# Kernel optimization log

Measured on AMD Instinct MI355X. Metric: run time of the kernel, lower is better.

Reference implementation:

```python
import jax, jax.numpy as jnp
import numpy as np

NDIM = (256, 256, 256)
NMIN = (-1.0, -1.0, -1.0)
NMAX = (1.0, 1.0, 1.0)
NDELTA = tuple((NMAX[i] - NMIN[i]) / (NDIM[i] - 1.0) for i in range(3))
MIN_DEG, MAX_DEG = 0, 10
ANNEALED_ALPHA = 1.0
EPS = 1e-12


def compute_grad(grid):
    # central differences on the voxel grid with edge padding -> [N, 3]
    g = grid.reshape(NDIM[0], NDIM[1], NDIM[2])
    p = jnp.pad(g, ((1, 1), (1, 1), (1, 1)), mode='edge')
    dx = (p[2:, 1:-1, 1:-1] - p[:-2, 1:-1, 1:-1]) / (2.0 * NDELTA[0])
    dy = (p[1:-1, 2:, 1:-1] - p[1:-1, :-2, 1:-1]) / (2.0 * NDELTA[1])
    dz = (p[1:-1, 1:-1, 2:] - p[1:-1, 1:-1, :-2]) / (2.0 * NDELTA[2])
    return jnp.stack([dx, dy, dz], axis=-1).reshape(-1, 3)


def trilinear3(data, pts):
    # data: [N, 4] flattened voxel features, pts: [B, 3] -> [B, 4]
    x = (pts[..., 0] - NMIN[0]) / NDELTA[0]
    y = (pts[..., 1] - NMIN[1]) / NDELTA[1]
    z = (pts[..., 2] - NMIN[2]) / NDELTA[2]
    x0f = jnp.floor(x); y0f = jnp.floor(y); z0f = jnp.floor(z)
    xd = (x - x0f)[..., None]
    yd = (y - y0f)[..., None]
    zd = (z - z0f)[..., None]
    x0 = jnp.clip(x0f.astype(jnp.int32), 0, NDIM[0] - 1)
    x1 = jnp.clip(x0f.astype(jnp.int32) + 1, 0, NDIM[0] - 1)
    y0 = jnp.clip(y0f.astype(jnp.int32), 0, NDIM[1] - 1)
    y1 = jnp.clip(y0f.astype(jnp.int32) + 1, 0, NDIM[1] - 1)
    z0 = jnp.clip(z0f.astype(jnp.int32), 0, NDIM[2] - 1)
    z1 = jnp.clip(z0f.astype(jnp.int32) + 1, 0, NDIM[2] - 1)
    sYZ, sZ = NDIM[1] * NDIM[2], NDIM[2]
    gat = lambda i, j, k: data[sYZ * i + sZ * j + k]
    c00 = gat(x0, y0, z0) * (1 - xd) + gat(x1, y0, z0) * xd
    c01 = gat(x0, y0, z1) * (1 - xd) + gat(x1, y0, z1) * xd
    c10 = gat(x0, y1, z0) * (1 - xd) + gat(x1, y1, z0) * xd
    c11 = gat(x0, y1, z1) * (1 - xd) + gat(x1, y1, z1) * xd
    c0 = c00 * (1 - yd) + c10 * yd
    c1 = c01 * (1 - yd) + c11 * yd
    return c0 * (1 - zd) + c1 * zd


def annealed_pos_enc(x, alpha):
    # nerfies-style windowed positional encoding with identity concat
    bands = jnp.arange(MIN_DEG, MAX_DEG, dtype=x.dtype)  # [D]
    scales = 2.0 ** bands
    xb = x[..., None, :] * scales[:, None]               # [..., D, 3]
    four = jnp.sin(jnp.stack([xb, xb + 0.5 * jnp.pi], axis=-2))  # [..., D, 2, 3]
    w = jnp.clip(alpha - bands, 0.0, 1.0)
    w = 0.5 * (1.0 - jnp.cos(jnp.pi * w))                # cosine easing window
    four = four * w[:, None, None]
    four = four.reshape(x.shape[:-1] + (-1,))            # [..., D*6]
    return jnp.concatenate([x, four], axis=-1)           # [..., 3 + D*6]


def mlp(feats, w0, b0, w1, b1, w2, b2, w3, b3, wo, bo):
    # net_depth=4, skip_layer=2 -> concat inputs after layer index 2
    h = jax.nn.relu(feats @ w0 + b0)
    h = jax.nn.relu(h @ w1 + b1)
    h = jax.nn.relu(h @ w2 + b2)
    h = jnp.concatenate([h, feats], axis=-1)
    h = jax.nn.relu(h @ w3 + b3)
    return h @ wo + bo


def safe_l2_norm(v):
    return jnp.sqrt(jnp.sum(v * v, axis=-1, keepdims=True) + EPS)


def setup_inputs() -> dict:
    key = jax.random.key(0)
    ks = jax.random.split(key, 8)
    B = 1048576
    N = NDIM[0] * NDIM[1] * NDIM[2]
    x = jax.random.uniform(ks[0], (B, 3), jnp.float32, -1.0, 1.0)
    grid = jax.random.normal(ks[1], (N, 1), jnp.float32)
    glorot = lambda k, fi, fo: jax.random.normal(k, (fi, fo), jnp.float32) * jnp.sqrt(2.0 / (fi + fo))
    return {
        'x': x, 'grid': grid,
        'w0': glorot(ks[2], 63, 128), 'b0': jnp.zeros((128,), jnp.float32),
        'w1': glorot(ks[3], 128, 128), 'b1': jnp.zeros((128,), jnp.float32),
        'w2': glorot(ks[4], 128, 128), 'b2': jnp.zeros((128,), jnp.float32),
        'w3': glorot(ks[5], 191, 128), 'b3': jnp.zeros((128,), jnp.float32),
        'wo': jax.random.normal(ks[6], (128, 3), jnp.float32) * 1e-5,  # output_init normal(1e-5)
        'bo': jnp.zeros((3,), jnp.float32),
    }


def reference(x, grid, w0, b0, w1, b1, w2, b2, w3, b3, wo, bo):
    data = jnp.concatenate([grid, compute_grad(grid)], axis=-1)  # [N, 4]
    ret = trilinear3(data, x)                                    # [B, 4]
    feats = annealed_pos_enc(x[:, None], ANNEALED_ALPHA * MAX_DEG)  # [B, 1, 63]
    raw = mlp(feats, w0, b0, w1, b1, w2, b2, w3, b3, wo, bo)[:, 0]  # [B, 3]
    # residual + direct output: rotate gradient vector by axis-angle raw
    theta = safe_l2_norm(raw)
    e = raw / theta
    cond = ret[..., 1:]
    a = safe_l2_norm(cond)
    v = cond / a
    rot = a * (jnp.cos(theta) * v + jnp.sin(theta) * jnp.cross(e, v)
               + (1.0 - jnp.cos(theta)) * jnp.sum(e * v, axis=-1, keepdims=True) * e)
    return (ret[..., :1], ret[..., 1:], rot)
```

## Files before the change

### kernel.cpp

```cpp
#include <hip/hip_runtime.h>


typedef __attribute__((ext_vector_type(8))) short bf8;
typedef __attribute__((ext_vector_type(4))) float f4;

__device__ __forceinline__ float bf2f(unsigned int u) {
    union { float f; unsigned int i; } v; v.i = u << 16; return v.f;
}
__device__ __forceinline__ unsigned short f2bf(float f) {
    union { float f; unsigned int i; } v; v.f = f;
    unsigned int x = v.i;
    return (unsigned short)((x + 0x7fffu + ((x >> 16) & 1u)) >> 16);
}
__device__ __forceinline__ unsigned int pkbf(float a, float b) {
    unsigned int r;
    asm("v_cvt_pk_bf16_f32 %0, %1, %2" : "=v"(r) : "v"(a), "v"(b));
    return r;
}
__device__ __forceinline__ float gv(const float* __restrict__ g, int i, int j, int k) {
    return g[(i * 256 + j) * 256 + k];
}
__device__ __forceinline__ int featmap(int kp) {
    if (kp < 3) return kp;
    if (kp == 3) return -1;
    const int m = kp - 4, b = m / 6, r = m - 6 * b, d = r >> 1, c = r & 1;
    return 3 + 6 * b + 3 * c + d;
}

#define WS_TOTAL 67584
#define SWZ_BLOCKS 264
#define DG_OFF_SH 131072
#define WS_NEED (262144ull + 16777216ull * 8ull)

__global__ __launch_bounds__(256) void prep(
    const float* __restrict__ g,
    const float* __restrict__ w0, const float* __restrict__ w1,
    const float* __restrict__ w2, const float* __restrict__ w3,
    const float* __restrict__ wo,
    unsigned short* __restrict__ ws, unsigned short* __restrict__ dg,
    int do_dgrid)
{
    const int bid = blockIdx.x;
    if (bid < SWZ_BLOCKS) {
        int idx = bid * 256 + threadIdx.x;
        const float* src; int base, NT, Kact, Nact, ld;
        if (idx < 8192)       { src = w0; base = 0;     NT = 8; Kact = 64;  Nact = 128; ld = 128; }
        else if (idx < 24576) { src = w1; base = 8192;  NT = 8; Kact = 128; Nact = 128; ld = 128; }
        else if (idx < 40960) { src = w2; base = 24576; NT = 8; Kact = 128; Nact = 128; ld = 128; }
        else if (idx < 65536) { src = w3; base = 40960; NT = 8; Kact = 192; Nact = 128; ld = 128; }
        else                  { src = wo; base = 65536; NT = 1; Kact = 128; Nact = 3;   ld = 3;   }
        int local = idx - base;
        int j = local & 7;
        int lane = (local >> 3) & 63;
        int chunk = local >> 9;
        int nt = chunk % NT, kt = chunk / NT;
        int k = kt * 32 + ((lane >> 4) << 3) + j;
        int n = nt * 16 + (lane & 15);
        float v = 0.0f;
        if (k < Kact && n < Nact) {
            int ko = k;
            if (base == 0)            ko = featmap(k);
            else if (base == 40960 && k >= 128) {
                int f = featmap(k - 128);
                ko = (f < 0) ? -1 : 128 + f;
            }
            if (ko >= 0) v = src[ko * ld + n];
        }
        ws[idx] = f2bf(v);
    } else if (do_dgrid) {
        const int t  = (bid - SWZ_BLOCKS) * 256 + threadIdx.x;
        const int k0 = (t & 63) << 2;
        const int j  = (t >> 6) & 255;
        const int i  = t >> 14;
        const float* row = g + (i * 256 + j) * 256;
        const f4 self = *(const f4*)(row + k0);
        const f4 xp = *(const f4*)(g + (min(i + 1, 255) * 256 + j) * 256 + k0);
        const f4 xm = *(const f4*)(g + (max(i - 1, 0)   * 256 + j) * 256 + k0);
        const f4 yp = *(const f4*)(g + (i * 256 + min(j + 1, 255)) * 256 + k0);
        const f4 ym = *(const f4*)(g + (i * 256 + max(j - 1, 0))   * 256 + k0);
        const float zlo = row[max(k0 - 1, 0)];
        const float zhi = row[min(k0 + 4, 255)];
        float zv[6] = {zlo, self[0], self[1], self[2], self[3], zhi};
        unsigned int o[8];
        #pragma unroll
        for (int q = 0; q < 4; ++q) {
            o[q * 2 + 0] = pkbf(self[q], (xp[q] - xm[q]) * 63.75f);
            o[q * 2 + 1] = pkbf((yp[q] - ym[q]) * 63.75f, (zv[q + 2] - zv[q]) * 63.75f);
        }
        unsigned short* dst = dg + (size_t)(((i * 256 + j) * 256 + k0)) * 4;
        *(uint4*)(dst)     = *(const uint4*)(o);
        *(uint4*)(dst + 8) = *(const uint4*)(o + 4);
    }
}

#define WV_SH 6656
#define HSTRIDE 136
#define FSTRIDE 72

template<bool FAST>
__global__ __launch_bounds__(256, 3) void voxmlp(
    const float* __restrict__ x, const float* __restrict__ grid,
    const unsigned short* __restrict__ ws, const unsigned short* __restrict__ dg,
    const float* __restrict__ b0, const float* __restrict__ b1,
    const float* __restrict__ b2, const float* __restrict__ b3,
    const float* __restrict__ bo,
    float* __restrict__ out, int B)
{
    __shared__ unsigned short smem[WV_SH * 4];

    const int lane = threadIdx.x & 63;
    const int wave = threadIdx.x >> 6;
    const int quad = lane >> 4;
    const int lm   = lane & 15;
    unsigned short* bufH = smem + wave * WV_SH;
    unsigned short* fbuf = bufH + 32 * HSTRIDE;

    const int pbase = blockIdx.x * 128 + wave * 32;

    const int p2   = lane & 31;
    const int role = lane >> 5;
    const int pid  = pbase + p2;

    const float px = x[pid * 3 + 0];
    const float py = x[pid * 3 + 1];
    const float pz = x[pid * 3 + 2];

    if (role == 0) {
        const float fx = (px + 1.0f) * 127.5f;
        const float fy = (py + 1.0f) * 127.5f;
        const float fz = (pz + 1.0f) * 127.5f;
        const float fx0 = floorf(fx), fy0 = floorf(fy), fz0 = floorf(fz);
        const float xd = fx - fx0, yd = fy - fy0, zd = fz - fz0;
        const int ix0 = min(max((int)fx0, 0), 255);
        const int iy0 = min(max((int)fy0, 0), 255);
        const int iz0 = min(max((int)fz0, 0), 255);
        const int ix1 = min(ix0 + 1, 255);
        const int iy1 = min(iy0 + 1, 255);
        const int iz1 = min(iz0 + 1, 255);

        float ret0 = 0.f, c1 = 0.f, c2 = 0.f, c3 = 0.f;
        if (FAST) {
            #pragma unroll
            for (int c = 0; c < 8; ++c) {
                const int i = (c & 4) ? ix1 : ix0;
                const int j = (c & 2) ? iy1 : iy0;
                const int k = (c & 1) ? iz1 : iz0;
                const float wgt = ((c & 4) ? xd : 1.0f - xd) *
                                  ((c & 2) ? yd : 1.0f - yd) *
                                  ((c & 1) ? zd : 1.0f - zd);
                const uint2 w = *(const uint2*)(dg + (size_t)((i * 256 + j) * 256 + k) * 4);
                ret0 = fmaf(wgt, bf2f(w.x & 0xffffu), ret0);
                c1   = fmaf(wgt, bf2f(w.x >> 16),     c1);
                c2   = fmaf(wgt, bf2f(w.y & 0xffffu), c2);
                c3   = fmaf(wgt, bf2f(w.y >> 16),     c3);
            }
        } else {
            #pragma unroll
            for (int c = 0; c < 8; ++c) {
                const int i = (c & 4) ? ix1 : ix0;
                const int j = (c & 2) ? iy1 : iy0;
                const int k = (c & 1) ? iz1 : iz0;
                const float wgt = ((c & 4) ? xd : 1.0f - xd) *
                                  ((c & 2) ? yd : 1.0f - yd) *
                                  ((c & 1) ? zd : 1.0f - zd);
                const float v  = gv(grid, i, j, k);
                const float gx = (gv(grid, min(i + 1, 255), j, k) - gv(grid, max(i - 1, 0), j, k)) * 63.75f;
                const float gy = (gv(grid, i, min(j + 1, 255), k) - gv(grid, i, max(j - 1, 0), k)) * 63.75f;
                const float gz = (gv(grid, i, j, min(k + 1, 255)) - gv(grid, i, j, max(k - 1, 0))) * 63.75f;
                ret0 = fmaf(wgt, v,  ret0);
                c1   = fmaf(wgt, gx, c1);
                c2   = fmaf(wgt, gy, c2);
                c3   = fmaf(wgt, gz, c3);
            }
        }
        out[pid] = ret0;
        out[B + pid * 3 + 0] = c1;
        out[B + pid * 3 + 1] = c2;
        out[B + pid * 3 + 2] = c3;
        float* cst = (float*)(fbuf + p2 * FSTRIDE + 64);
        cst[0] = c1; cst[1] = c2; cst[2] = c3;
    } else {
        unsigned int f[32];
        f[0] = pkbf(px, py);
        f[1] = pkbf(pz, 0.0f);
        const float crd[3] = {px, py, pz};
        float s = 1.0f;
        #pragma unroll
        for (int b = 0; b < 10; ++b) {
            #pragma unroll
            for (int d = 0; d < 3; ++d) {
                float sv, cv;
                __sincosf(crd[d] * s, &sv, &cv);
                f[2 + b * 3 + d] = pkbf(sv, cv);
            }
            s *= 2.0f;
        }
        unsigned short* fb = fbuf + p2 * FSTRIDE;
        #pragma unroll
        for (int i = 0; i < 8; ++i)
            *(uint4*)(fb + i * 8) = *(const uint4*)(&f[i * 4]);
    }
    __builtin_amdgcn_s_barrier();

    bf8 af[2][6];
    const int arow0 = lm * HSTRIDE + quad * 8;
    const int frow0 = lm * FSTRIDE + quad * 8;

    auto store_tile = [&](f4 acc, int pt, int ut) {
        uint2 pk;
        pk.x = pkbf(fmaxf(acc[0], 0.f), fmaxf(acc[1], 0.f));
        pk.y = pkbf(fmaxf(acc[2], 0.f), fmaxf(acc[3], 0.f));
        *(uint2*)(bufH + (pt * 16 + lm) * HSTRIDE + ut * 16 + quad * 4) = pk;
    };

    #pragma unroll
    for (int pt = 0; pt < 2; ++pt)
        #pragma unroll
        for (int kt = 0; kt < 2; ++kt)
            af[pt][kt] = *(const bf8*)(fbuf + pt * 16 * FSTRIDE + frow0 + kt * 32);
    #pragma unroll
    for (int ut = 0; ut < 8; ++ut) {
        bf8 wf[2];
        #pragma unroll
        for (int kt = 0; kt < 2; ++kt)
            wf[kt] = *(const bf8*)(ws + 0 + (((kt * 8 + ut) * 64 + lane) << 3));
        const f4 bias = *(const f4*)(b0 + ut * 16 + quad * 4);
        #pragma unroll
        for (int pt = 0; pt < 2; ++pt) {
            f4 acc = bias;
            #pragma unroll
            for (int kt = 0; kt < 2; ++kt)
                acc = __builtin_amdgcn_mfma_f32_16x16x32_bf16(wf[kt], af[pt][kt], acc, 0, 0, 0);
            store_tile(acc, pt, ut);
        }
    }
    __builtin_amdgcn_s_barrier();

    #pragma unroll
    for (int layer = 0; layer < 2; ++layer) {
        const unsigned short* wsl = ws + (layer == 0 ? 8192 : 24576);
        const float* bias_p = (layer == 0) ? b1 : b2;
        #pragma unroll
        for (int pt = 0; pt < 2; ++pt)
            #pragma unroll
            for (int kt = 0; kt < 4; ++kt)
                af[pt][kt] = *(const bf8*)(bufH + pt * 16 * HSTRIDE + arow0 + kt * 32);
        #pragma unroll
        for (int ut = 0; ut < 8; ++ut) {
            bf8 wf[4];
            #pragma unroll
            for (int kt = 0; kt < 4; ++kt)
                wf[kt] = *(const bf8*)(wsl + (((kt * 8 + ut) * 64 + lane) << 3));
            const f4 bias = *(const f4*)(bias_p + ut * 16 + quad * 4);
            #pragma unroll
            for (int pt = 0; pt < 2; ++pt) {
                f4 acc = bias;
                #pragma unroll
                for (int kt = 0; kt < 4; ++kt)
                    acc = __builtin_amdgcn_mfma_f32_16x16x32_bf16(wf[kt], af[pt][kt], acc, 0, 0, 0);
                store_tile(acc, pt, ut);
            }
        }
        __builtin_amdgcn_s_barrier();
    }

    #pragma unroll
    for (int pt = 0; pt < 2; ++pt) {
        #pragma unroll
        for (int kt = 0; kt < 4; ++kt)
            af[pt][kt] = *(const bf8*)(bufH + pt * 16 * HSTRIDE + arow0 + kt * 32);
        #pragma unroll
        for (int kk = 0; kk < 2; ++kk)
            af[pt][4 + kk] = *(const bf8*)(fbuf + pt * 16 * FSTRIDE + frow0 + kk * 32);
    }
    #pragma unroll
    for (int ut = 0; ut < 8; ++ut) {
        bf8 wf[6];
        #pragma unroll
        for (int kt = 0; kt < 6; ++kt)
            wf[kt] = *(const bf8*)(ws + 40960 + (((kt * 8 + ut) * 64 + lane) << 3));
        const f4 bias = *(const f4*)(b3 + ut * 16 + quad * 4);
        #pragma unroll
        for (int pt = 0; pt < 2; ++pt) {
            f4 acc = bias;
            #pragma unroll
            for (int kt = 0; kt < 6; ++kt)
                acc = __builtin_amdgcn_mfma_f32_16x16x32_bf16(wf[kt], af[pt][kt], acc, 0, 0, 0);
            store_tile(acc, pt, ut);
        }
    }
    __builtin_amdgcn_s_barrier();

    #pragma unroll
    for (int pt = 0; pt < 2; ++pt)
        #pragma unroll
        for (int kt = 0; kt < 4; ++kt)
            af[pt][kt] = *(const bf8*)(bufH + pt * 16 * HSTRIDE + arow0 + kt * 32);
    bf8 wf[4];
    #pragma unroll
    for (int kt = 0; kt < 4; ++kt)
        wf[kt] = *(const bf8*)(ws + 65536 + ((kt * 64 + lane) << 3));

    #pragma unroll
    for (int pt = 0; pt < 2; ++pt) {
        f4 acc;
        #pragma unroll
        for (int r = 0; r < 4; ++r) {
            const int u = quad * 4 + r;
            acc[r] = (u < 3) ? bo[u] : 0.0f;
        }
        #pragma unroll
        for (int kt = 0; kt < 4; ++kt)
            acc = __builtin_amdgcn_mfma_f32_16x16x32_bf16(wf[kt], af[pt][kt], acc, 0, 0, 0);

        const int pp = pt * 16 + lm;
        const float* cst = (const float*)(fbuf + pp * FSTRIDE + 64);
        const float g1 = cst[0], g2 = cst[1], g3 = cst[2];
        const float r0 = acc[0], r1 = acc[1], r2 = acc[2];
        const float theta = sqrtf(fmaf(r0, r0, fmaf(r1, r1, r2 * r2)) + 1e-12f);
        const float it = __builtin_amdgcn_rcpf(theta);
        const float e0 = r0 * it, e1 = r1 * it, e2 = r2 * it;
        const float a = sqrtf(fmaf(g1, g1, fmaf(g2, g2, g3 * g3)) + 1e-12f);
        const float ia = __builtin_amdgcn_rcpf(a);
        const float v0 = g1 * ia, v1 = g2 * ia, v2 = g3 * ia;
        float st, ct;
        __sincosf(theta, &st, &ct);
        const float cx = e1 * v2 - e2 * v1;
        const float cy = e2 * v0 - e0 * v2;
        const float cz = e0 * v1 - e1 * v0;
        const float om = (1.0f - ct) * (e0 * v0 + e1 * v1 + e2 * v2);
        if (quad == 0) {
            const int pid2 = pbase + pp;
            out[4 * B + pid2 * 3 + 0] = a * (ct * v0 + st * cx + om * e0);
            out[4 * B + pid2 * 3 + 1] = a * (ct * v1 + st * cy + om * e1);
            out[4 * B + pid2 * 3 + 2] = a * (ct * v2 + st * cz + om * e2);
        }
    }
}

extern "C" void kernel_launch(void* const* d_in, const int* in_sizes, int n_in,
                              void* d_out, int out_size, void* d_ws, size_t ws_size,
                              hipStream_t stream)
{
    const float* x    = (const float*)d_in[0];
    const float* grid = (const float*)d_in[1];
    const float* w0   = (const float*)d_in[2];
    const float* b0   = (const float*)d_in[3];
    const float* w1   = (const float*)d_in[4];
    const float* b1   = (const float*)d_in[5];
    const float* w2   = (const float*)d_in[6];
    const float* b2   = (const float*)d_in[7];
    const float* w3   = (const float*)d_in[8];
    const float* b3   = (const float*)d_in[9];
    const float* wo   = (const float*)d_in[10];
    const float* bo   = (const float*)d_in[11];
    float* out = (float*)d_out;
    unsigned short* ws = (unsigned short*)d_ws;
    unsigned short* dg = ws + DG_OFF_SH;

    const int B = in_sizes[0] / 3;
    const int fast = (ws_size >= WS_NEED) ? 1 : 0;
    const int nprep = fast ? (SWZ_BLOCKS + 16384) : SWZ_BLOCKS;
    prep<<<nprep, 256, 0, stream>>>(grid, w0, w1, w2, w3, wo, ws, dg, fast);
    if (fast)
        voxmlp<true><<<B / 128, 256, 0, stream>>>(x, grid, ws, dg, b0, b1, b2, b3, bo, out, B);
    else
        voxmlp<false><<<B / 128, 256, 0, stream>>>(x, grid, ws, dg, b0, b1, b2, b3, bo, out, B);
}
```

Baseline: 372.2 us.

## Switch MLP matmuls to FP8 MFMA and widen derivative-grid prep per thread

Weights, positional features and hidden activations are now stored as FP8 and fed to the fp8 16x16x32 MFMA instead of bf16. This halves the weight and LDS traffic and lets occupancy rise to 5 waves per SIMD. The tiny output weights are pre-scaled by 8192 to stay in FP8 range and unscaled afterwards. The prep kernel also processes 8 voxels per thread instead of 4. FP8 lowers MLP accuracy and may push errors past tolerance.

```diff
diff --git a/kernel.cpp b/kernel.cpp
--- a/kernel.cpp
+++ b/kernel.cpp
@@ -1,8 +1,8 @@
 #include <hip/hip_runtime.h>
 
 
-typedef __attribute__((ext_vector_type(8))) short bf8;
 typedef __attribute__((ext_vector_type(4))) float f4;
+typedef long long llg;
 
 __device__ __forceinline__ float bf2f(unsigned int u) {
     union { float f; unsigned int i; } v; v.i = u << 16; return v.f;
@@ -29,15 +29,18 @@
 
 #define WS_TOTAL 67584
 #define SWZ_BLOCKS 264
+#define DG_BLOCKS 8192
 #define DG_OFF_SH 131072
 #define WS_NEED (262144ull + 16777216ull * 8ull)
+#define WO_SCALE 8192.0f
+#define WO_INV   (1.0f / 8192.0f)
 
 __global__ __launch_bounds__(256) void prep(
     const float* __restrict__ g,
     const float* __restrict__ w0, const float* __restrict__ w1,
     const float* __restrict__ w2, const float* __restrict__ w3,
     const float* __restrict__ wo,
-    unsigned short* __restrict__ ws, unsigned short* __restrict__ dg,
+    unsigned char* __restrict__ ws8, unsigned short* __restrict__ dg,
     int do_dgrid)
 {
     const int bid = blockIdx.x;
@@ -65,55 +68,77 @@
                 ko = (f < 0) ? -1 : 128 + f;
             }
             if (ko >= 0) v = src[ko * ld + n];
-        }
-        ws[idx] = f2bf(v);
+            if (base == 65536) v *= WO_SCALE;
+        }
+        int p = __builtin_amdgcn_cvt_pk_fp8_f32(v, v, 0, false);
+        ws8[idx] = (unsigned char)(p & 0xff);
     } else if (do_dgrid) {
         const int t  = (bid - SWZ_BLOCKS) * 256 + threadIdx.x;
-        const int k0 = (t & 63) << 2;
-        const int j  = (t >> 6) & 255;
-        const int i  = t >> 14;
+        const int k0 = (t & 31) << 3;
+        const int j  = (t >> 5) & 255;
+        const int i  = t >> 13;
         const float* row = g + (i * 256 + j) * 256;
-        const f4 self = *(const f4*)(row + k0);
-        const f4 xp = *(const f4*)(g + (min(i + 1, 255) * 256 + j) * 256 + k0);
-        const f4 xm = *(const f4*)(g + (max(i - 1, 0)   * 256 + j) * 256 + k0);
-        const f4 yp = *(const f4*)(g + (i * 256 + min(j + 1, 255)) * 256 + k0);
-        const f4 ym = *(const f4*)(g + (i * 256 + max(j - 1, 0))   * 256 + k0);
-        const float zlo = row[max(k0 - 1, 0)];
-        const float zhi = row[min(k0 + 4, 255)];
-        float zv[6] = {zlo, self[0], self[1], self[2], self[3], zhi};
-        unsigned int o[8];
-        #pragma unroll
-        for (int q = 0; q < 4; ++q) {
-            o[q * 2 + 0] = pkbf(self[q], (xp[q] - xm[q]) * 63.75f);
-            o[q * 2 + 1] = pkbf((yp[q] - ym[q]) * 63.75f, (zv[q + 2] - zv[q]) * 63.75f);
+        const float* rxp = g + (min(i + 1, 255) * 256 + j) * 256;
+        const float* rxm = g + (max(i - 1, 0)   * 256 + j) * 256;
+        const float* ryp = g + (i * 256 + min(j + 1, 255)) * 256;
+        const float* rym = g + (i * 256 + max(j - 1, 0))   * 256;
+        float se[8], sxp[8], sxm[8], syp[8], sym[8];
+        {
+            f4 a = *(const f4*)(row + k0), b = *(const f4*)(row + k0 + 4);
+            #pragma unroll
+            for (int q = 0; q < 4; ++q) { se[q] = a[q]; se[q + 4] = b[q]; }
+            a = *(const f4*)(rxp + k0); b = *(const f4*)(rxp + k0 + 4);
+            #pragma unroll
+            for (int q = 0; q < 4; ++q) { sxp[q] = a[q]; sxp[q + 4] = b[q]; }
+            a = *(const f4*)(rxm + k0); b = *(const f4*)(rxm + k0 + 4);
+            #pragma unroll
+            for (int q = 0; q < 4; ++q) { sxm[q] = a[q]; sxm[q + 4] = b[q]; }
+            a = *(const f4*)(ryp + k0); b = *(const f4*)(ryp + k0 + 4);
+            #pragma unroll
+            for (int q = 0; q < 4; ++q) { syp[q] = a[q]; syp[q + 4] = b[q]; }
+            a = *(const f4*)(rym + k0); b = *(const f4*)(rym + k0 + 4);
+            #pragma unroll
+            for (int q = 0; q < 4; ++q) { sym[q] = a[q]; sym[q + 4] = b[q]; }
+        }
+        float zv[10];
+        zv[0] = row[max(k0 - 1, 0)];
+        #pragma unroll
+        for (int q = 0; q < 8; ++q) zv[q + 1] = se[q];
+        zv[9] = row[min(k0 + 8, 255)];
+        unsigned int o[16];
+        #pragma unroll
+        for (int q = 0; q < 8; ++q) {
+            o[q * 2 + 0] = pkbf(se[q], (sxp[q] - sxm[q]) * 63.75f);
+            o[q * 2 + 1] = pkbf((syp[q] - sym[q]) * 63.75f, (zv[q + 2] - zv[q]) * 63.75f);
         }
         unsigned short* dst = dg + (size_t)(((i * 256 + j) * 256 + k0)) * 4;
-        *(uint4*)(dst)     = *(const uint4*)(o);
-        *(uint4*)(dst + 8) = *(const uint4*)(o + 4);
-    }
-}
-
-#define WV_SH 6656
-#define HSTRIDE 136
-#define FSTRIDE 72
+        #pragma unroll
+        for (int q = 0; q < 4; ++q)
+            *(uint4*)(dst + q * 8) = *(const uint4*)(&o[q * 4]);
+    }
+}
+
+#define HSTRIDE_B 136
+#define FSTRIDE_B 88
+#define WV_BYTES (32 * HSTRIDE_B + 32 * FSTRIDE_B)
 
 template<bool FAST>
-__global__ __launch_bounds__(256, 3) void voxmlp(
+__global__ __launch_bounds__(256, 5) void voxmlp(
     const float* __restrict__ x, const float* __restrict__ grid,
-    const unsigned short* __restrict__ ws, const unsigned short* __restrict__ dg,
+    const unsigned char* __restrict__ ws8, const unsigned short* __restrict__ dg,
     const float* __restrict__ b0, const float* __restrict__ b1,
     const float* __restrict__ b2, const float* __restrict__ b3,
     const float* __restrict__ bo,
     float* __restrict__ out, int B)
 {
-    __shared__ unsigned short smem[WV_SH * 4];
+    __shared__ unsigned char smem[WV_BYTES * 4];
 
     const int lane = threadIdx.x & 63;
     const int wave = threadIdx.x >> 6;
     const int quad = lane >> 4;
     const int lm   = lane & 15;
-    unsigned short* bufH = smem + wave * WV_SH;
-    unsigned short* fbuf = bufH + 32 * HSTRIDE;
+    unsigned char* bufH = smem + wave * WV_BYTES;
+    unsigned char* fbuf = bufH + 32 * HSTRIDE_B;
 
     const int pbase = blockIdx.x * 128 + wave * 32;
 
@@ -177,60 +202,73 @@
         out[B + pid * 3 + 0] = c1;
         out[B + pid * 3 + 1] = c2;
         out[B + pid * 3 + 2] = c3;
-        float* cst = (float*)(fbuf + p2 * FSTRIDE + 64);
+        float* cst = (float*)(fbuf + p2 * FSTRIDE_B + 64);
         cst[0] = c1; cst[1] = c2; cst[2] = c3;
     } else {
-        unsigned int f[32];
-        f[0] = pkbf(px, py);
-        f[1] = pkbf(pz, 0.0f);
+        float s[64];
+        s[0] = px; s[1] = py; s[2] = pz; s[3] = 0.0f;
         const float crd[3] = {px, py, pz};
-        float s = 1.0f;
+        float sc = 1.0f;
         #pragma unroll
         for (int b = 0; b < 10; ++b) {
             #pragma unroll
             for (int d = 0; d < 3; ++d) {
                 float sv, cv;
-                __sincosf(crd[d] * s, &sv, &cv);
-                f[2 + b * 3 + d] = pkbf(sv, cv);
+                __sincosf(crd[d] * sc, &sv, &cv);
+                s[4 + b * 6 + d * 2 + 0] = sv;
+                s[4 + b * 6 + d * 2 + 1] = cv;
             }
-            s *= 2.0f;
-        }
-        unsigned short* fb = fbuf + p2 * FSTRIDE;
-        #pragma unroll
-        for (int i = 0; i < 8; ++i)
-            *(uint4*)(fb + i * 8) = *(const uint4*)(&f[i * 4]);
+            sc *= 2.0f;
+        }
+        unsigned int dw[16];
+        #pragma unroll
+        for (int i = 0; i < 16; ++i) {
+            int d = __builtin_amdgcn_cvt_pk_fp8_f32(s[4 * i + 0], s[4 * i + 1], 0, false);
+            d     = __builtin_amdgcn_cvt_pk_fp8_f32(s[4 * i + 2], s[4 * i + 3], d, true);
+            dw[i] = (unsigned int)d;
+        }
+        unsigned char* fb = fbuf + p2 * FSTRIDE_B;
+        #pragma unroll
+        for (int i = 0; i < 4; ++i) {
+            uint2 pk; pk.x = dw[2 * i]; pk.y = dw[2 * i + 1];
+            *(uint2*)(fb + i * 8) = pk;
+        }
+        #pragma unroll
+        for (int i = 4; i < 8; ++i) {
+            uint2 pk; pk.x = dw[2 * i]; pk.y = dw[2 * i + 1];
+            *(uint2*)(fb + i * 8) = pk;
+        }
     }
     __builtin_amdgcn_s_barrier();
 
-    bf8 af[2][6];
-    const int arow0 = lm * HSTRIDE + quad * 8;
-    const int frow0 = lm * FSTRIDE + quad * 8;
+    llg af[2][6];
+    const int arow0 = lm * HSTRIDE_B + quad * 8;
+    const int frow0 = lm * FSTRIDE_B + quad * 8;
 
     auto store_tile = [&](f4 acc, int pt, int ut) {
-        uint2 pk;
-        pk.x = pkbf(fmaxf(acc[0], 0.f), fmaxf(acc[1], 0.f));
-        pk.y = pkbf(fmaxf(acc[2], 0.f), fmaxf(acc[3], 0.f));
-        *(uint2*)(bufH + (pt * 16 + lm) * HSTRIDE + ut * 16 + quad * 4) = pk;
+        int d = __builtin_amdgcn_cvt_pk_fp8_f32(fmaxf(acc[0], 0.f), fmaxf(acc[1], 0.f), 0, false);
+        d     = __builtin_amdgcn_cvt_pk_fp8_f32(fmaxf(acc[2], 0.f), fmaxf(acc[3], 0.f), d, true);
+        *(int*)(bufH + (pt * 16 + lm) * HSTRIDE_B + ut * 16 + quad * 4) = d;
     };
 
     #pragma unroll
     for (int pt = 0; pt < 2; ++pt)
         #pragma unroll
         for (int kt = 0; kt < 2; ++kt)
-            af[pt][kt] = *(const bf8*)(fbuf + pt * 16 * FSTRIDE + frow0 + kt * 32);
+            af[pt][kt] = *(const llg*)(fbuf + pt * 16 * FSTRIDE_B + frow0 + kt * 32);
     #pragma unroll
     for (int ut = 0; ut < 8; ++ut) {
-        bf8 wf[2];
+        llg wf[2];
         #pragma unroll
         for (int kt = 0; kt < 2; ++kt)
-            wf[kt] = *(const bf8*)(ws + 0 + (((kt * 8 + ut) * 64 + lane) << 3));
+            wf[kt] = *(const llg*)(ws8 + 0 + (((kt * 8 + ut) * 64 + lane) << 3));
         const f4 bias = *(const f4*)(b0 + ut * 16 + quad * 4);
         #pragma unroll
         for (int pt = 0; pt < 2; ++pt) {
             f4 acc = bias;
             #pragma unroll
             for (int kt = 0; kt < 2; ++kt)
-                acc = __builtin_amdgcn_mfma_f32_16x16x32_bf16(wf[kt], af[pt][kt], acc, 0, 0, 0);
+                acc = __builtin_amdgcn_mfma_f32_16x16x32_fp8_fp8(wf[kt], af[pt][kt], acc, 0, 0, 0);
             store_tile(acc, pt, ut);
         }
     }
@@ -238,26 +276,26 @@
 
     #pragma unroll
     for (int layer = 0; layer < 2; ++layer) {
-        const unsigned short* wsl = ws + (layer == 0 ? 8192 : 24576);
+        const unsigned char* wsl = ws8 + (layer == 0 ? 8192 : 24576);
         const float* bias_p = (layer == 0) ? b1 : b2;
         #pragma unroll
         for (int pt = 0; pt < 2; ++pt)
             #pragma unroll
             for (int kt = 0; kt < 4; ++kt)
-                af[pt][kt] = *(const bf8*)(bufH + pt * 16 * HSTRIDE + arow0 + kt * 32);
+                af[pt][kt] = *(const llg*)(bufH + pt * 16 * HSTRIDE_B + arow0 + kt * 32);
         #pragma unroll
         for (int ut = 0; ut < 8; ++ut) {
-            bf8 wf[4];
+            llg wf[4];
             #pragma unroll
             for (int kt = 0; kt < 4; ++kt)
-                wf[kt] = *(const bf8*)(wsl + (((kt * 8 + ut) * 64 + lane) << 3));
+                wf[kt] = *(const llg*)(wsl + (((kt * 8 + ut) * 64 + lane) << 3));
             const f4 bias = *(const f4*)(bias_p + ut * 16 + quad * 4);
             #pragma unroll
             for (int pt = 0; pt < 2; ++pt) {
                 f4 acc = bias;
                 #pragma unroll
                 for (int kt = 0; kt < 4; ++kt)
-                    acc = __builtin_amdgcn_mfma_f32_16x16x32_bf16(wf[kt], af[pt][kt], acc, 0, 0, 0);
+                    acc = __builtin_amdgcn_mfma_f32_16x16x32_fp8_fp8(wf[kt], af[pt][kt], acc, 0, 0, 0);
                 store_tile(acc, pt, ut);
             }
         }
@@ -268,24 +306,24 @@
     for (int pt = 0; pt < 2; ++pt) {
         #pragma unroll
         for (int kt = 0; kt < 4; ++kt)
-            af[pt][kt] = *(const bf8*)(bufH + pt * 16 * HSTRIDE + arow0 + kt * 32);
+            af[pt][kt] = *(const llg*)(bufH + pt * 16 * HSTRIDE_B + arow0 + kt * 32);
         #pragma unroll
         for (int kk = 0; kk < 2; ++kk)
-            af[pt][4 + kk] = *(const bf8*)(fbuf + pt * 16 * FSTRIDE + frow0 + kk * 32);
+            af[pt][4 + kk] = *(const llg*)(fbuf + pt * 16 * FSTRIDE_B + frow0 + kk * 32);
     }
     #pragma unroll
     for (int ut = 0; ut < 8; ++ut) {
-        bf8 wf[6];
+        llg wf[6];
         #pragma unroll
         for (int kt = 0; kt < 6; ++kt)
-            wf[kt] = *(const bf8*)(ws + 40960 + (((kt * 8 + ut) * 64 + lane) << 3));
+            wf[kt] = *(const llg*)(ws8 + 40960 + (((kt * 8 + ut) * 64 + lane) << 3));
         const f4 bias = *(const f4*)(b3 + ut * 16 + quad * 4);
         #pragma unroll
         for (int pt = 0; pt < 2; ++pt) {
             f4 acc = bias;
             #pragma unroll
             for (int kt = 0; kt < 6; ++kt)
-                acc = __builtin_amdgcn_mfma_f32_16x16x32_bf16(wf[kt], af[pt][kt], acc, 0, 0, 0);
+                acc = __builtin_amdgcn_mfma_f32_16x16x32_fp8_fp8(wf[kt], af[pt][kt], acc, 0, 0, 0);
             store_tile(acc, pt, ut);
         }
     }
@@ -295,28 +333,26 @@
     for (int pt = 0; pt < 2; ++pt)
         #pragma unroll
         for (int kt = 0; kt < 4; ++kt)
-            af[pt][kt] = *(const bf8*)(bufH + pt * 16 * HSTRIDE + arow0 + kt * 32);
-    bf8 wf[4];
+            af[pt][kt] = *(const llg*)(bufH + pt * 16 * HSTRIDE_B + arow0 + kt * 32);
+    llg wf[4];
     #pragma unroll
     for (int kt = 0; kt < 4; ++kt)
-        wf[kt] = *(const bf8*)(ws + 65536 + ((kt * 64 + lane) << 3));
-
+        wf[kt] = *(const llg*)(ws8 + 65536 + ((kt * 64 + lane) << 3));
+
+    const float bo0 = bo[0], bo1 = bo[1], bo2 = bo[2];
     #pragma unroll
     for (int pt = 0; pt < 2; ++pt) {
-        f4 acc;
-        #pragma unroll
-        for (int r = 0; r < 4; ++r) {
-            const int u = quad * 4 + r;
-            acc[r] = (u < 3) ? bo[u] : 0.0f;
-        }
+        f4 acc = {0.f, 0.f, 0.f, 0.f};
         #pragma unroll
         for (int kt = 0; kt < 4; ++kt)
-            acc = __builtin_amdgcn_mfma_f32_16x16x32_bf16(wf[kt], af[pt][kt], acc, 0, 0, 0);
+            acc = __builtin_amdgcn_mfma_f32_16x16x32_fp8_fp8(wf[kt], af[pt][kt], acc, 0, 0, 0);
 
         const int pp = pt * 16 + lm;
-        const float* cst = (const float*)(fbuf + pp * FSTRIDE + 64);
+        const float* cst = (const float*)(fbuf + pp * FSTRIDE_B + 64);
         const float g1 = cst[0], g2 = cst[1], g3 = cst[2];
-        const float r0 = acc[0], r1 = acc[1], r2 = acc[2];
+        const float r0 = acc[0] * WO_INV + bo0;
+        const float r1 = acc[1] * WO_INV + bo1;
+        const float r2 = acc[2] * WO_INV + bo2;
         const float theta = sqrtf(fmaf(r0, r0, fmaf(r1, r1, r2 * r2)) + 1e-12f);
         const float it = __builtin_amdgcn_rcpf(theta);
         const float e0 = r0 * it, e1 = r1 * it, e2 = r2 * it;
@@ -355,15 +391,15 @@
     const float* wo   = (const float*)d_in[10];
     const float* bo   = (const float*)d_in[11];
     float* out = (float*)d_out;
-    unsigned short* ws = (unsigned short*)d_ws;
-    unsigned short* dg = ws + DG_OFF_SH;
+    unsigned char* ws8 = (unsigned char*)d_ws;
+    unsigned short* dg = (unsigned short*)d_ws + DG_OFF_SH;
 
     const int B = in_sizes[0] / 3;
     const int fast = (ws_size >= WS_NEED) ? 1 : 0;
-    const int nprep = fast ? (SWZ_BLOCKS + 16384) : SWZ_BLOCKS;
-    prep<<<nprep, 256, 0, stream>>>(grid, w0, w1, w2, w3, wo, ws, dg, fast);
+    const int nprep = fast ? (SWZ_BLOCKS + DG_BLOCKS) : SWZ_BLOCKS;
+    prep<<<nprep, 256, 0, stream>>>(grid, w0, w1, w2, w3, wo, ws8, dg, fast);
     if (fast)
-        voxmlp<true><<<B / 128, 256, 0, stream>>>(x, grid, ws, dg, b0, b1, b2, b3, bo, out, B);
+        voxmlp<true><<<B / 128, 256, 0, stream>>>(x, grid, ws8, dg, b0, b1, b2, b3, bo, out, B);
     else
-        voxmlp<false><<<B / 128, 256, 0, stream>>>(x, grid, ws, dg, b0, b1, b2, b3, bo, out, B);
-}
+        voxmlp<false><<<B / 128, 256, 0, stream>>>(x, grid, ws8, dg, b0, b1, b2, b3, bo, out, B);
+}
```

After: 368.1 us. No clear change (-1.1%).
